# Kernel optimization log

Hardware: AMD Instinct MI355X
Metric: run time of the kernel (lower is better)

## Reference

```python
import jax, jax.numpy as jnp
import numpy as np

B, N, D = 16, 1024, 16  # graphs, nodes, embedding_dim


def setup_inputs() -> dict:
    key = jax.random.key(0)
    ks = jax.random.split(key, 13)
    s = 0.05  # small weight scale to keep exp(alpha) well-behaved
    return {
        "X": jax.random.normal(ks[0], (B, N, D), dtype=jnp.float32),
        "init_param": jax.random.normal(ks[1], (2,), dtype=jnp.float32) * s,
        "Wq": jax.random.normal(ks[2], (D - 1, D, D), dtype=jnp.float32) * s,
        "bq": jax.random.normal(ks[3], (D - 1, D), dtype=jnp.float32) * s,
        "Wk": jax.random.normal(ks[4], (D - 1, D, D), dtype=jnp.float32) * s,
        "bk": jax.random.normal(ks[5], (D - 1, D), dtype=jnp.float32) * s,
        "Wv": jax.random.normal(ks[6], (D - 1, D, D), dtype=jnp.float32) * s,
        "bv": jax.random.normal(ks[7], (D - 1, D), dtype=jnp.float32) * s,
        "Wo": jax.random.normal(ks[8], (D - 1, D, D), dtype=jnp.float32) * s,
        "bo": jax.random.normal(ks[9], (D - 1, D), dtype=jnp.float32) * s,
        "Wf": jax.random.normal(ks[10], (D - 1, 2, D), dtype=jnp.float32) * s,
        "bf": jax.random.normal(ks[11], (D - 1, 2), dtype=jnp.float32) * s,
    }


def reference(X, init_param, Wq, bq, Wk, bk, Wv, bv, Wo, bo, Wf, bf):
    b, n, d = X.shape
    dt = X.dtype
    Zs = []
    logdet = jnp.zeros((b, n), dt)
    for i in range(d):
        if i == 0:
            mu, alpha = init_param[0], init_param[1]
        else:
            l = i - 1
            Xi = X[:, :, :i]  # [B,N,i] growing ragged slice
            Q = Xi @ Wq[l, :i, :i].T + bq[l, :i]
            K = Xi @ Wk[l, :i, :i].T + bk[l, :i]
            V = Xi @ Wv[l, :i, :i].T + bv[l, :i]
            # SAB/MAB: softmax(QK^T / sqrt(dim_V=i)); num_heads=1
            A = jax.nn.softmax(
                jnp.einsum("bnd,bmd->bnm", Q, K) / jnp.sqrt(jnp.asarray(i, dt)),
                axis=-1,
            )  # [B,N,N]
            O = Q + jnp.einsum("bnm,bmd->bnd", A, V)
            O = O + jax.nn.relu(O @ Wo[l, :i, :i].T + bo[l, :i])
            out = O @ Wf[l, :, :i].T + bf[l]  # [B,N,2]
            mu, alpha = out[..., 0], out[..., 1]
        Zs.append((X[:, :, i] - mu) / jnp.exp(alpha))
        logdet = logdet - alpha
    Z = jnp.stack(Zs, axis=-1)
    return Z, logdet
```

## Files before the change

kernel.cpp:

```cpp
#include <hip/hip_runtime.h>
#include <math.h>

#define Bb 16
#define Nn 1024
#define Dd 16
#define NL 15

typedef __attribute__((ext_vector_type(8))) short short8;
typedef __attribute__((ext_vector_type(4))) float f32x4;

#if __has_builtin(__builtin_amdgcn_exp2f)
#define EXP2(x) __builtin_amdgcn_exp2f(x)
#else
#define EXP2(x) exp2f(x)
#endif

#define PROW 40
#define WREG (64 * PROW * 2)
#define V_OFF (Nn * 16 * 2)
#define VSTR 1032
#define P_OFF (V_OFF + Dd * VSTR * 2)
#define LDS_TOTAL (P_OFF + 16 * WREG)

__device__ __forceinline__ unsigned pack2bf(float a, float b) {
    unsigned ua = __float_as_uint(a) + 0x8000u;
    unsigned ub = __float_as_uint(b) + 0x8000u;
    return (ua >> 16) | (ub & 0xffff0000u);
}
__device__ __forceinline__ unsigned short bf1(float a) {
    return (unsigned short)((__float_as_uint(a) + 0x8000u) >> 16);
}

__device__ __forceinline__ void project(const float* __restrict__ xrow,
                                        const float* __restrict__ W,
                                        const float* __restrict__ bias,
                                        int i, float* __restrict__ q) {
#pragma unroll
    for (int r = 0; r < 16; r++) q[r] = 0.f;
    for (int c = 0; c < i; c++) {
        float xc = xrow[c];
#pragma unroll
        for (int r = 0; r < 16; r++) q[r] = fmaf(xc, W[r * 16 + c], q[r]);
    }
#pragma unroll
    for (int r = 0; r < 16; r++) q[r] = (r < i) ? (q[r] + bias[r]) : 0.f;
}

__device__ __forceinline__ void load_row16(const float* __restrict__ p, float* __restrict__ x) {
    const float4* xp = (const float4*)p;
    float4 a = xp[0], b = xp[1], c = xp[2], d = xp[3];
    x[0]=a.x; x[1]=a.y; x[2]=a.z; x[3]=a.w;
    x[4]=b.x; x[5]=b.y; x[6]=b.z; x[7]=b.w;
    x[8]=c.x; x[9]=c.y; x[10]=c.z; x[11]=c.w;
    x[12]=d.x; x[13]=d.y; x[14]=d.z; x[15]=d.w;
}

__global__ void gf_init(const float* __restrict__ X, const float* __restrict__ ip,
                        float* __restrict__ out) {
    int idx = blockIdx.x * blockDim.x + threadIdx.x;
    if (idx >= Bb * Nn) return;
    float mu = ip[0], alpha = ip[1];
    float x0 = X[(size_t)idx * Dd];
    out[(size_t)idx * Dd] = (x0 - mu) * __expf(-alpha);
    out[(size_t)Bb * Nn * Dd + idx] = -alpha;
}

__launch_bounds__(1024, 4)
__global__ void gf_fused(const float* __restrict__ X,
                         const float* __restrict__ Wq, const float* __restrict__ bq,
                         const float* __restrict__ Wk, const float* __restrict__ bk,
                         const float* __restrict__ Wv, const float* __restrict__ bv,
                         const float* __restrict__ Wo, const float* __restrict__ bo,
                         const float* __restrict__ Wf, const float* __restrict__ bf,
                         float* __restrict__ out) {
    extern __shared__ char smem[];
    const int l = blockIdx.x, b = blockIdx.y, i = l + 1;
    const int t = threadIdx.x;
    const int wid = t >> 6, lane = t & 63;
    const int c15 = lane & 15, quad = lane >> 4;
    const float qscale = 1.4426950408889634f * rsqrtf((float)i);

    unsigned short* Ksh = (unsigned short*)smem;
    unsigned short* Vsh = (unsigned short*)(smem + V_OFF);
    unsigned short* Pw  = (unsigned short*)(smem + P_OFF + wid * WREG);

    const float* Xb  = X  + (size_t)b * Nn * Dd;
    const float* wq  = Wq + l * 256;  const float* bql = bq + l * 16;
    const float* wk  = Wk + l * 256;  const float* bkl = bk + l * 16;
    const float* wvp = Wv + l * 256;  const float* bvl = bv + l * 16;
    const float* wo  = Wo + l * 256;  const float* bol = bo + l * 16;
    const float* wf  = Wf + l * 32;   const float* bfl = bf + l * 2;

    {
        float xr[16]; load_row16(Xb + (size_t)t * Dd, xr);
        float tmp[16];
        unsigned u[8];

        project(xr, wk, bkl, i, tmp);
#pragma unroll
        for (int r = 0; r < 8; r++) u[r] = pack2bf(tmp[2*r], tmp[2*r+1]);
        {
            uint4* kd = (uint4*)(Ksh + t * 16);
            kd[0] = make_uint4(u[0], u[1], u[2], u[3]);
            kd[1] = make_uint4(u[4], u[5], u[6], u[7]);
        }

        project(xr, wvp, bvl, i, tmp);
#pragma unroll
        for (int d = 0; d < 16; d++) Vsh[d * VSTR + t] = bf1(tmp[d]);

        project(xr, wq, bql, i, tmp);
#pragma unroll
        for (int r = 0; r < 8; r++) u[r] = pack2bf(tmp[2*r] * qscale, tmp[2*r+1] * qscale);
        {
            uint4* qd = (uint4*)(Pw + lane * PROW);
            qd[0] = make_uint4(u[0], u[1], u[2], u[3]);
            qd[1] = make_uint4(u[4], u[5], u[6], u[7]);
        }
    }
    __syncthreads();

    short8 zr = {0,0,0,0,0,0,0,0};
    f32x4 zf = {0.f,0.f,0.f,0.f};

    short8 qf[4];
#pragma unroll
    for (int f = 0; f < 4; f++)
        qf[f] = (quad < 2) ? *(const short8*)(Pw + (f*16 + c15) * PROW + quad * 8) : zr;

    f32x4 ot[4] = {zf, zf, zf, zf};
    float rs[4] = {0.f, 0.f, 0.f, 0.f};

    const unsigned short* Kp = Ksh + (size_t)c15 * 16 + quad * 8;
    const unsigned short* Vp = Vsh + (size_t)c15 * VSTR + quad * 8;

    for (int kb = 0; kb < Nn; kb += 32) {
        short8 kf[2];
#pragma unroll
        for (int kt = 0; kt < 2; kt++)
            kf[kt] = (quad < 2) ? *(const short8*)(Kp + (size_t)(kb + kt*16) * 16) : zr;

        f32x4 st[2][4];
#pragma unroll
        for (int kt = 0; kt < 2; kt++)
#pragma unroll
            for (int f = 0; f < 4; f++)
                st[kt][f] = __builtin_amdgcn_mfma_f32_16x16x32_bf16(kf[kt], qf[f], zf, 0, 0, 0);

#pragma unroll
        for (int kt = 0; kt < 2; kt++)
#pragma unroll
            for (int f = 0; f < 4; f++) {
                float p0 = EXP2(st[kt][f].x), p1 = EXP2(st[kt][f].y);
                float p2 = EXP2(st[kt][f].z), p3 = EXP2(st[kt][f].w);
                rs[f] += (p0 + p1) + (p2 + p3);
                *(uint2*)(Pw + (f*16 + c15) * PROW + kt*16 + quad*4) =
                    make_uint2(pack2bf(p0, p1), pack2bf(p2, p3));
            }

        short8 vf = *(const short8*)(Vp + kb);
#pragma unroll
        for (int f = 0; f < 4; f++) {
            short8 pf = *(const short8*)(Pw + (f*16 + c15) * PROW + quad * 8);
            ot[f] = __builtin_amdgcn_mfma_f32_16x16x32_bf16(vf, pf, ot[f], 0, 0, 0);
        }
    }

    float* Ow = (float*)Pw;
#pragma unroll
    for (int f = 0; f < 4; f++) {
        float r = rs[f];
        r += __shfl_xor(r, 16);
        r += __shfl_xor(r, 32);
        float inv = 1.f / r;
        f32x4 res;
        res.x = ot[f].x * inv; res.y = ot[f].y * inv;
        res.z = ot[f].z * inv; res.w = ot[f].w * inv;
        *(f32x4*)(Ow + (f*16 + c15) * 20 + quad * 4) = res;
    }

    {
        float xr[16]; load_row16(Xb + (size_t)t * Dd, xr);
        float q[16];  project(xr, wq, bql, i, q);
        const float* orow = (const float*)(smem + P_OFF + wid * WREG) + lane * 20;

        float a[16];
#pragma unroll
        for (int c = 0; c < 16; c++) a[c] = q[c] + orow[c];

        float tt[16];
#pragma unroll
        for (int r = 0; r < 16; r++) {
            float acc = bol[r];
#pragma unroll
            for (int c = 0; c < 16; c++) acc = fmaf(a[c], wo[r * 16 + c], acc);
            tt[r] = fmaxf(acc, 0.f);
        }
#pragma unroll
        for (int r = 0; r < 16; r++) a[r] += (r < i) ? tt[r] : 0.f;

        float mu = bfl[0], al = bfl[1];
#pragma unroll
        for (int c = 0; c < 16; c++) {
            mu = fmaf(a[c], wf[c], mu);
            al = fmaf(a[c], wf[16 + c], al);
        }
        out[((size_t)(b * Nn + t)) * Dd + i] = (xr[i] - mu) * __expf(-al);
        atomicAdd(out + (size_t)Bb * Nn * Dd + b * Nn + t, -al);
    }
}

__launch_bounds__(512, 2)
__global__ void gf_layer_fb(const float* __restrict__ X,
                            const float* __restrict__ Wq, const float* __restrict__ bq,
                            const float* __restrict__ Wk, const float* __restrict__ bk,
                            const float* __restrict__ Wv, const float* __restrict__ bv,
                            const float* __restrict__ Wo, const float* __restrict__ bo,
                            const float* __restrict__ Wf, const float* __restrict__ bf,
                            float* __restrict__ out) {
    const int l = blockIdx.x, b = blockIdx.y, i = l + 1, t = threadIdx.x;
    const float rscale = rsqrtf((float)i);
    __shared__ float Ksh[512 * 16];
    __shared__ float Vsh[512 * 16];
    const float* Xb = X + (size_t)b * Nn * Dd;
    const float* wq = Wq + l * 256; const float* wk = Wk + l * 256;
    const float* wv = Wv + l * 256; const float* wo = Wo + l * 256;
    const float* wf = Wf + l * 32;
    const float* bql = bq + l * 16; const float* bkl = bk + l * 16;
    const float* bvl = bv + l * 16; const float* bol = bo + l * 16;
    const float* bfl = bf + l * 2;
    const int n0 = t, n1 = t + 512;
    float q0[16], q1[16], xi0, xi1;
    {
        float xr[16];
        load_row16(Xb + (size_t)n0 * Dd, xr); xi0 = xr[i]; project(xr, wq, bql, i, q0);
        load_row16(Xb + (size_t)n1 * Dd, xr); xi1 = xr[i]; project(xr, wq, bql, i, q1);
    }
    float o0[16], o1[16];
#pragma unroll
    for (int c = 0; c < 16; c++) { o0[c] = 0.f; o1[c] = 0.f; }
    float ls0 = 0.f, ls1 = 0.f;
    for (int ch = 0; ch < 2; ch++) {
        float kr[16], vr[16];
        {
            float kx[16];
            load_row16(Xb + (size_t)(ch * 512 + t) * Dd, kx);
            project(kx, wk, bkl, i, kr);
            project(kx, wv, bvl, i, vr);
        }
        __syncthreads();
#pragma unroll
        for (int j = 0; j < 4; j++) {
            ((float4*)&Ksh[t * 16])[j] = ((float4*)kr)[j];
            ((float4*)&Vsh[t * 16])[j] = ((float4*)vr)[j];
        }
        __syncthreads();
        for (int k = 0; k < 512; k++) {
            float kk[16], vv[16];
#pragma unroll
            for (int j = 0; j < 4; j++) ((float4*)kk)[j] = ((const float4*)&Ksh[k * 16])[j];
            float s0 = 0.f, s1 = 0.f;
#pragma unroll
            for (int c = 0; c < 16; c++) { s0 = fmaf(q0[c], kk[c], s0); s1 = fmaf(q1[c], kk[c], s1); }
            float p0 = __expf(s0 * rscale), p1 = __expf(s1 * rscale);
            ls0 += p0; ls1 += p1;
#pragma unroll
            for (int j = 0; j < 4; j++) ((float4*)vv)[j] = ((const float4*)&Vsh[k * 16])[j];
#pragma unroll
            for (int c = 0; c < 16; c++) { o0[c] = fmaf(p0, vv[c], o0[c]); o1[c] = fmaf(p1, vv[c], o1[c]); }
        }
        __syncthreads();
    }
    float* logdet = out + (size_t)Bb * Nn * Dd;
#pragma unroll
    for (int rowsel = 0; rowsel < 2; rowsel++) {
        const float* qr = rowsel ? q1 : q0; const float* orr = rowsel ? o1 : o0;
        float lsum = rowsel ? ls1 : ls0; float xin = rowsel ? xi1 : xi0;
        int n = rowsel ? n1 : n0;
        float a[16]; float inv = 1.f / lsum;
#pragma unroll
        for (int c = 0; c < 16; c++) a[c] = qr[c] + orr[c] * inv;
        float tt[16];
#pragma unroll
        for (int r = 0; r < 16; r++) {
            float acc = bol[r];
#pragma unroll
            for (int c = 0; c < 16; c++) acc = fmaf(a[c], wo[r * 16 + c], acc);
            tt[r] = fmaxf(acc, 0.f);
        }
#pragma unroll
        for (int r = 0; r < 16; r++) a[r] += (r < i) ? tt[r] : 0.f;
        float mu = bfl[0], al = bfl[1];
#pragma unroll
        for (int c = 0; c < 16; c++) { mu = fmaf(a[c], wf[c], mu); al = fmaf(a[c], wf[16 + c], al); }
        out[((size_t)(b * Nn + n)) * Dd + i] = (xin - mu) * __expf(-al);
        atomicAdd(logdet + b * Nn + n, -al);
    }
}

extern "C" void kernel_launch(void* const* d_in, const int* in_sizes, int n_in,
                              void* d_out, int out_size, void* d_ws, size_t ws_size,
                              hipStream_t stream) {
    const float* X  = (const float*)d_in[0];
    const float* ip = (const float*)d_in[1];
    const float* Wq = (const float*)d_in[2];
    const float* bq = (const float*)d_in[3];
    const float* Wk = (const float*)d_in[4];
    const float* bk = (const float*)d_in[5];
    const float* Wv = (const float*)d_in[6];
    const float* bv = (const float*)d_in[7];
    const float* Wo = (const float*)d_in[8];
    const float* bo = (const float*)d_in[9];
    const float* Wf = (const float*)d_in[10];
    const float* bf = (const float*)d_in[11];
    float* out = (float*)d_out;

    gf_init<<<(Bb * Nn + 255) / 256, 256, 0, stream>>>(X, ip, out);

    hipError_t e = hipFuncSetAttribute((const void*)gf_fused,
                                       hipFuncAttributeMaxDynamicSharedMemorySize,
                                       LDS_TOTAL);
    if (e == hipSuccess) {
        gf_fused<<<dim3(NL, Bb), 1024, LDS_TOTAL, stream>>>(
            X, Wq, bq, Wk, bk, Wv, bv, Wo, bo, Wf, bf, out);
    } else {
        gf_layer_fb<<<dim3(NL, Bb), 512, 0, stream>>>(
            X, Wq, bq, Wk, bk, Wv, bv, Wo, bo, Wf, bf, out);
    }
}
```

Before: 158.4 us.

## Use 32x32 MFMA for scores, prefetch K/V, replace atomics with workspace reduction

The QK^T score computation moves from eight 16x16x32 MFMAs per tile, half of which ran on zero-padded operands, to two 32x32x16 MFMAs that match the real head dimension of 16 and avoid the wasted padding. K and V fragments for the next tile are now prefetched in registers, and the V stride changes. Per-layer alphas are written to a workspace and summed by a new final kernel, replacing the init kernel plus contended atomicAdds on logdet. This adds an extra kernel launch, uses workspace memory, and changes how the row-sum shuffles are reduced.

```diff
diff --git a/kernel.cpp b/kernel.cpp
--- a/kernel.cpp
+++ b/kernel.cpp
@@ -8,6 +8,7 @@
 
 typedef __attribute__((ext_vector_type(8))) short short8;
 typedef __attribute__((ext_vector_type(4))) float f32x4;
+typedef __attribute__((ext_vector_type(16))) float f32x16;
 
 #if __has_builtin(__builtin_amdgcn_exp2f)
 #define EXP2(x) __builtin_amdgcn_exp2f(x)
@@ -15,10 +16,10 @@
 #define EXP2(x) exp2f(x)
 #endif
 
-#define PROW 40
-#define WREG (64 * PROW * 2)
-#define V_OFF (Nn * 16 * 2)
-#define VSTR 1032
+#define VSTR 1040
+#define PSTR 40
+#define WREG (64 * PSTR * 2)
+#define V_OFF (Nn * Dd * 2)
 #define P_OFF (V_OFF + Dd * VSTR * 2)
 #define LDS_TOTAL (P_OFF + 16 * WREG)
 
@@ -53,6 +54,170 @@
     x[4]=b.x; x[5]=b.y; x[6]=b.z; x[7]=b.w;
     x[8]=c.x; x[9]=c.y; x[10]=c.z; x[11]=c.w;
     x[12]=d.x; x[13]=d.y; x[14]=d.z; x[15]=d.w;
+}
+
+__launch_bounds__(1024, 4)
+__global__ void gf_fused(const float* __restrict__ X,
+                         const float* __restrict__ Wq, const float* __restrict__ bq,
+                         const float* __restrict__ Wk, const float* __restrict__ bk,
+                         const float* __restrict__ Wv, const float* __restrict__ bv,
+                         const float* __restrict__ Wo, const float* __restrict__ bo,
+                         const float* __restrict__ Wf, const float* __restrict__ bf,
+                         float* __restrict__ als, float* __restrict__ out) {
+    extern __shared__ char smem[];
+    const int l = blockIdx.x, b = blockIdx.y, i = l + 1;
+    const int t = threadIdx.x;
+    const int wid = t >> 6, lane = t & 63;
+    const int c15 = lane & 15, quad = lane >> 4;
+    const int q31 = lane & 31, h = lane >> 5;
+    const float qscale = 1.4426950408889634f * rsqrtf((float)i);
+
+    unsigned short* Ksh = (unsigned short*)smem;
+    unsigned short* Vsh = (unsigned short*)(smem + V_OFF);
+    unsigned short* Pw  = (unsigned short*)(smem + P_OFF + wid * WREG);
+
+    const float* Xb  = X  + (size_t)b * Nn * Dd;
+    const float* wq  = Wq + l * 256;  const float* bql = bq + l * 16;
+    const float* wk  = Wk + l * 256;  const float* bkl = bk + l * 16;
+    const float* wvp = Wv + l * 256;  const float* bvl = bv + l * 16;
+    const float* wo  = Wo + l * 256;  const float* bol = bo + l * 16;
+    const float* wf  = Wf + l * 32;   const float* bfl = bf + l * 2;
+
+    {
+        float xr[16]; load_row16(Xb + (size_t)t * Dd, xr);
+        float tmp[16];
+        unsigned u[8];
+
+        project(xr, wk, bkl, i, tmp);
+#pragma unroll
+        for (int r = 0; r < 8; r++) u[r] = pack2bf(tmp[2*r], tmp[2*r+1]);
+        {
+            uint4* kd = (uint4*)(Ksh + t * 16);
+            kd[0] = make_uint4(u[0], u[1], u[2], u[3]);
+            kd[1] = make_uint4(u[4], u[5], u[6], u[7]);
+        }
+
+        project(xr, wvp, bvl, i, tmp);
+#pragma unroll
+        for (int d = 0; d < 16; d++) Vsh[d * VSTR + t] = bf1(tmp[d]);
+
+        project(xr, wq, bql, i, tmp);
+#pragma unroll
+        for (int r = 0; r < 8; r++) u[r] = pack2bf(tmp[2*r] * qscale, tmp[2*r+1] * qscale);
+        {
+            uint4* qd = (uint4*)(Pw + lane * PSTR);
+            qd[0] = make_uint4(u[0], u[1], u[2], u[3]);
+            qd[1] = make_uint4(u[4], u[5], u[6], u[7]);
+        }
+    }
+    __syncthreads();
+
+    f32x16 zf16 = {};
+    f32x4  zf4  = {};
+
+    short8 qf[2];
+    qf[0] = *(const short8*)(Pw + q31        * PSTR + h * 8);
+    qf[1] = *(const short8*)(Pw + (32 + q31) * PSTR + h * 8);
+
+    const unsigned short* Kp = Ksh + (size_t)q31 * 16 + h * 8;
+    const unsigned short* Vp = Vsh + (size_t)c15 * VSTR + quad * 8;
+
+    f32x4 ot[4] = {zf4, zf4, zf4, zf4};
+    float rs[2] = {0.f, 0.f};
+
+    short8 kf = *(const short8*)(Kp);
+    short8 vf = *(const short8*)(Vp);
+
+    for (int kb = 0; kb < Nn; kb += 32) {
+        const int kn = (kb + 32) & (Nn - 1);
+        short8 kfn = *(const short8*)(Kp + (size_t)kn * 16);
+        short8 vfn = *(const short8*)(Vp + kn);
+
+        f32x16 st0 = __builtin_amdgcn_mfma_f32_32x32x16_bf16(kf, qf[0], zf16, 0, 0, 0);
+        f32x16 st1 = __builtin_amdgcn_mfma_f32_32x32x16_bf16(kf, qf[1], zf16, 0, 0, 0);
+
+        unsigned short* pw0 = Pw + q31 * PSTR + 4 * h;
+#pragma unroll
+        for (int g = 0; g < 4; g++) {
+            float e0 = EXP2(st0[4*g+0]), e1 = EXP2(st0[4*g+1]);
+            float e2 = EXP2(st0[4*g+2]), e3 = EXP2(st0[4*g+3]);
+            rs[0] += (e0 + e1) + (e2 + e3);
+            *(uint2*)(pw0 + 8*g) = make_uint2(pack2bf(e0, e1), pack2bf(e2, e3));
+        }
+        unsigned short* pw1 = pw0 + 32 * PSTR;
+#pragma unroll
+        for (int g = 0; g < 4; g++) {
+            float e0 = EXP2(st1[4*g+0]), e1 = EXP2(st1[4*g+1]);
+            float e2 = EXP2(st1[4*g+2]), e3 = EXP2(st1[4*g+3]);
+            rs[1] += (e0 + e1) + (e2 + e3);
+            *(uint2*)(pw1 + 8*g) = make_uint2(pack2bf(e0, e1), pack2bf(e2, e3));
+        }
+
+#pragma unroll
+        for (int f = 0; f < 4; f++) {
+            short8 pf = *(const short8*)(Pw + (f*16 + c15) * PSTR + quad * 8);
+            ot[f] = __builtin_amdgcn_mfma_f32_16x16x32_bf16(vf, pf, ot[f], 0, 0, 0);
+        }
+        kf = kfn; vf = vfn;
+    }
+
+    rs[0] += __shfl_xor(rs[0], 32);
+    rs[1] += __shfl_xor(rs[1], 32);
+    const float iv0 = 1.f / rs[0];
+    const float iv1 = 1.f / rs[1];
+
+    float* Ow = (float*)Pw;
+#pragma unroll
+    for (int f = 0; f < 4; f++) {
+        float iv = __shfl((f & 2) ? iv1 : iv0, (f & 1) * 16 + c15);
+        f32x4 res;
+        res.x = ot[f].x * iv; res.y = ot[f].y * iv;
+        res.z = ot[f].z * iv; res.w = ot[f].w * iv;
+        *(f32x4*)(Ow + (f*16 + c15) * 20 + quad * 4) = res;
+    }
+
+    {
+        float xr[16]; load_row16(Xb + (size_t)t * Dd, xr);
+        float q[16];  project(xr, wq, bql, i, q);
+        const float* orow = (const float*)(smem + P_OFF + wid * WREG) + lane * 20;
+
+        float a[16];
+#pragma unroll
+        for (int c = 0; c < 16; c++) a[c] = q[c] + orow[c];
+
+        float tt[16];
+#pragma unroll
+        for (int r = 0; r < 16; r++) {
+            float acc = bol[r];
+#pragma unroll
+            for (int c = 0; c < 16; c++) acc = fmaf(a[c], wo[r * 16 + c], acc);
+            tt[r] = fmaxf(acc, 0.f);
+        }
+#pragma unroll
+        for (int r = 0; r < 16; r++) a[r] += (r < i) ? tt[r] : 0.f;
+
+        float mu = bfl[0], al = bfl[1];
+#pragma unroll
+        for (int c = 0; c < 16; c++) {
+            mu = fmaf(a[c], wf[c], mu);
+            al = fmaf(a[c], wf[16 + c], al);
+        }
+        out[((size_t)(b * Nn + t)) * Dd + i] = (xr[i] - mu) * __expf(-al);
+        als[(size_t)l * (Bb * Nn) + b * Nn + t] = al;
+    }
+}
+
+__launch_bounds__(1024)
+__global__ void gf_final(const float* __restrict__ X, const float* __restrict__ ip,
+                         const float* __restrict__ als, float* __restrict__ out) {
+    const int idx = blockIdx.x * 1024 + threadIdx.x;
+    const float mu = ip[0], a0 = ip[1];
+    float x0 = X[(size_t)idx * Dd];
+    out[(size_t)idx * Dd] = (x0 - mu) * __expf(-a0);
+    float ld = -a0;
+#pragma unroll
+    for (int l = 0; l < NL; l++) ld -= als[(size_t)l * (Bb * Nn) + idx];
+    out[(size_t)Bb * Nn * Dd + idx] = ld;
 }
 
 __global__ void gf_init(const float* __restrict__ X, const float* __restrict__ ip,
@@ -63,151 +228,6 @@
     float x0 = X[(size_t)idx * Dd];
     out[(size_t)idx * Dd] = (x0 - mu) * __expf(-alpha);
     out[(size_t)Bb * Nn * Dd + idx] = -alpha;
-}
-
-__launch_bounds__(1024, 4)
-__global__ void gf_fused(const float* __restrict__ X,
-                         const float* __restrict__ Wq, const float* __restrict__ bq,
-                         const float* __restrict__ Wk, const float* __restrict__ bk,
-                         const float* __restrict__ Wv, const float* __restrict__ bv,
-                         const float* __restrict__ Wo, const float* __restrict__ bo,
-                         const float* __restrict__ Wf, const float* __restrict__ bf,
-                         float* __restrict__ out) {
-    extern __shared__ char smem[];
-    const int l = blockIdx.x, b = blockIdx.y, i = l + 1;
-    const int t = threadIdx.x;
-    const int wid = t >> 6, lane = t & 63;
-    const int c15 = lane & 15, quad = lane >> 4;
-    const float qscale = 1.4426950408889634f * rsqrtf((float)i);
-
-    unsigned short* Ksh = (unsigned short*)smem;
-    unsigned short* Vsh = (unsigned short*)(smem + V_OFF);
-    unsigned short* Pw  = (unsigned short*)(smem + P_OFF + wid * WREG);
-
-    const float* Xb  = X  + (size_t)b * Nn * Dd;
-    const float* wq  = Wq + l * 256;  const float* bql = bq + l * 16;
-    const float* wk  = Wk + l * 256;  const float* bkl = bk + l * 16;
-    const float* wvp = Wv + l * 256;  const float* bvl = bv + l * 16;
-    const float* wo  = Wo + l * 256;  const float* bol = bo + l * 16;
-    const float* wf  = Wf + l * 32;   const float* bfl = bf + l * 2;
-
-    {
-        float xr[16]; load_row16(Xb + (size_t)t * Dd, xr);
-        float tmp[16];
-        unsigned u[8];
-
-        project(xr, wk, bkl, i, tmp);
-#pragma unroll
-        for (int r = 0; r < 8; r++) u[r] = pack2bf(tmp[2*r], tmp[2*r+1]);
-        {
-            uint4* kd = (uint4*)(Ksh + t * 16);
-            kd[0] = make_uint4(u[0], u[1], u[2], u[3]);
-            kd[1] = make_uint4(u[4], u[5], u[6], u[7]);
-        }
-
-        project(xr, wvp, bvl, i, tmp);
-#pragma unroll
-        for (int d = 0; d < 16; d++) Vsh[d * VSTR + t] = bf1(tmp[d]);
-
-        project(xr, wq, bql, i, tmp);
-#pragma unroll
-        for (int r = 0; r < 8; r++) u[r] = pack2bf(tmp[2*r] * qscale, tmp[2*r+1] * qscale);
-        {
-            uint4* qd = (uint4*)(Pw + lane * PROW);
-            qd[0] = make_uint4(u[0], u[1], u[2], u[3]);
-            qd[1] = make_uint4(u[4], u[5], u[6], u[7]);
-        }
-    }
-    __syncthreads();
-
-    short8 zr = {0,0,0,0,0,0,0,0};
-    f32x4 zf = {0.f,0.f,0.f,0.f};
-
-    short8 qf[4];
-#pragma unroll
-    for (int f = 0; f < 4; f++)
-        qf[f] = (quad < 2) ? *(const short8*)(Pw + (f*16 + c15) * PROW + quad * 8) : zr;
-
-    f32x4 ot[4] = {zf, zf, zf, zf};
-    float rs[4] = {0.f, 0.f, 0.f, 0.f};
-
-    const unsigned short* Kp = Ksh + (size_t)c15 * 16 + quad * 8;
-    const unsigned short* Vp = Vsh + (size_t)c15 * VSTR + quad * 8;
-
-    for (int kb = 0; kb < Nn; kb += 32) {
-        short8 kf[2];
-#pragma unroll
-        for (int kt = 0; kt < 2; kt++)
-            kf[kt] = (quad < 2) ? *(const short8*)(Kp + (size_t)(kb + kt*16) * 16) : zr;
-
-        f32x4 st[2][4];
-#pragma unroll
-        for (int kt = 0; kt < 2; kt++)
-#pragma unroll
-            for (int f = 0; f < 4; f++)
-                st[kt][f] = __builtin_amdgcn_mfma_f32_16x16x32_bf16(kf[kt], qf[f], zf, 0, 0, 0);
-
-#pragma unroll
-        for (int kt = 0; kt < 2; kt++)
-#pragma unroll
-            for (int f = 0; f < 4; f++) {
-                float p0 = EXP2(st[kt][f].x), p1 = EXP2(st[kt][f].y);
-                float p2 = EXP2(st[kt][f].z), p3 = EXP2(st[kt][f].w);
-                rs[f] += (p0 + p1) + (p2 + p3);
-                *(uint2*)(Pw + (f*16 + c15) * PROW + kt*16 + quad*4) =
-                    make_uint2(pack2bf(p0, p1), pack2bf(p2, p3));
-            }
-
-        short8 vf = *(const short8*)(Vp + kb);
-#pragma unroll
-        for (int f = 0; f < 4; f++) {
-            short8 pf = *(const short8*)(Pw + (f*16 + c15) * PROW + quad * 8);
-            ot[f] = __builtin_amdgcn_mfma_f32_16x16x32_bf16(vf, pf, ot[f], 0, 0, 0);
-        }
-    }
-
-    float* Ow = (float*)Pw;
-#pragma unroll
-    for (int f = 0; f < 4; f++) {
-        float r = rs[f];
-        r += __shfl_xor(r, 16);
-        r += __shfl_xor(r, 32);
-        float inv = 1.f / r;
-        f32x4 res;
-        res.x = ot[f].x * inv; res.y = ot[f].y * inv;
-        res.z = ot[f].z * inv; res.w = ot[f].w * inv;
-        *(f32x4*)(Ow + (f*16 + c15) * 20 + quad * 4) = res;
-    }
-
-    {
-        float xr[16]; load_row16(Xb + (size_t)t * Dd, xr);
-        float q[16];  project(xr, wq, bql, i, q);
-        const float* orow = (const float*)(smem + P_OFF + wid * WREG) + lane * 20;
-
-        float a[16];
-#pragma unroll
-        for (int c = 0; c < 16; c++) a[c] = q[c] + orow[c];
-
-        float tt[16];
-#pragma unroll
-        for (int r = 0; r < 16; r++) {
-            float acc = bol[r];
-#pragma unroll
-            for (int c = 0; c < 16; c++) acc = fmaf(a[c], wo[r * 16 + c], acc);
-            tt[r] = fmaxf(acc, 0.f);
-        }
-#pragma unroll
-        for (int r = 0; r < 16; r++) a[r] += (r < i) ? tt[r] : 0.f;
-
-        float mu = bfl[0], al = bfl[1];
-#pragma unroll
-        for (int c = 0; c < 16; c++) {
-            mu = fmaf(a[c], wf[c], mu);
-            al = fmaf(a[c], wf[16 + c], al);
-        }
-        out[((size_t)(b * Nn + t)) * Dd + i] = (xr[i] - mu) * __expf(-al);
-        atomicAdd(out + (size_t)Bb * Nn * Dd + b * Nn + t, -al);
-    }
 }
 
 __launch_bounds__(512, 2)
@@ -315,15 +335,17 @@
     const float* bf = (const float*)d_in[11];
     float* out = (float*)d_out;
 
-    gf_init<<<(Bb * Nn + 255) / 256, 256, 0, stream>>>(X, ip, out);
-
+    const size_t need = (size_t)NL * Bb * Nn * sizeof(float);
     hipError_t e = hipFuncSetAttribute((const void*)gf_fused,
                                        hipFuncAttributeMaxDynamicSharedMemorySize,
                                        LDS_TOTAL);
-    if (e == hipSuccess) {
+    if (e == hipSuccess && ws_size >= need) {
+        float* als = (float*)d_ws;
         gf_fused<<<dim3(NL, Bb), 1024, LDS_TOTAL, stream>>>(
-            X, Wq, bq, Wk, bk, Wv, bv, Wo, bo, Wf, bf, out);
+            X, Wq, bq, Wk, bk, Wv, bv, Wo, bo, Wf, bf, als, out);
+        gf_final<<<Bb, 1024, 0, stream>>>(X, ip, als, out);
     } else {
+        gf_init<<<(Bb * Nn + 255) / 256, 256, 0, stream>>>(X, ip, out);
         gf_layer_fb<<<dim3(NL, Bb), 512, 0, stream>>>(
             X, Wq, bq, Wk, bk, Wv, bv, Wo, bo, Wf, bf, out);
     }
```

New measurement: 156.3 us. No clear change (-1.3%).
